# Kernel tuning notes

Hardware: AMD Instinct MI355X
Metric: run time of the kernel (lower is better)

The kernel has to match this reference:

```python
import jax, jax.numpy as jnp
import numpy as np

B, S, N = 128, 64, 32          # batch, self nodes, neighbors per node
INP_CAPS, OUT_CAPS, CAP_SZ = 8, 8, 16
K = OUT_CAPS
D = OUT_CAPS * CAP_SZ          # 128
C = D // K                     # capsule dim = 16
TAU = 1.0
EPS = 1e-12                    # F.normalize eps


def _l2norm(x):
    n = jnp.sqrt(jnp.sum(x * x, axis=-1, keepdims=True))
    return x / jnp.maximum(n, EPS)


def setup_inputs() -> dict:
    key = jax.random.key(0)
    k1, k2, k3, k4 = jax.random.split(key, 4)
    inp_d = INP_CAPS * CAP_SZ
    return {
        "self_vectors": jax.random.normal(k1, (B, S, inp_d), dtype=jnp.float32),
        "neighbor_vectors": jax.random.normal(k2, (B, S, N, inp_d), dtype=jnp.float32),
        "w1": jax.random.normal(k3, (inp_d, D), dtype=jnp.float32) * (1.0 / np.sqrt(inp_d)),
        "b1": jax.random.normal(k4, (D,), dtype=jnp.float32) * (1.0 / np.sqrt(D)),
        "max_iter": 3,
    }


def reference(self_vectors, neighbor_vectors, w1, b1, max_iter):
    inp_d = INP_CAPS * CAP_SZ
    self_z = jax.nn.relu(self_vectors.reshape(-1, inp_d) @ w1 + b1)
    neigh_z = jax.nn.relu(neighbor_vectors.reshape(-1, inp_d) @ w1 + b1)

    # [B,S,K,C] and [B,S,N,K,C], each capsule L2-normalized
    self_zn = _l2norm(self_z.reshape(B, S, K, C))
    neigh_zn = _l2norm(neigh_z.reshape(B, S, N, K, C))

    u = None
    for it in range(max_iter):
        if u is None:
            p = jnp.zeros((B, S, N, K), dtype=self_zn.dtype)
        else:
            # agreement scores: [B,S,N,K]
            p = jnp.einsum("bsnkc,bskc->bsnk", neigh_zn, u)
        p = jax.nn.softmax(p / TAU, axis=-1)
        # weighted neighbor sum over N -> [B,S,K,C]
        u = jnp.einsum("bsnkc,bsnk->bskc", neigh_zn, p) + self_zn
        if it < max_iter - 1:
            u = _l2norm(u)

    # dropout p=0.0 (eval) -> identity
    return jax.nn.relu(u.reshape(B, S, D))
```

## Files before the change

### kernel.cpp

```cpp
#include <hip/hip_runtime.h>
#include <hip/hip_bf16.h>


#define NB 32
#define DD 128
#define ZS 132
#define PPS 37
#define AST 136

#define SMEM_BYTES 20704
#define ALO_OFF_SH 4488
#define NRM_OFF_F 4488
#define PP_OFF_F 4752
#define UU_OFF_F 5048

typedef __attribute__((ext_vector_type(8))) short bf16x8;
typedef __attribute__((ext_vector_type(4))) float f32x4;
typedef __attribute__((ext_vector_type(4))) float float4v;
typedef __attribute__((ext_vector_type(2))) unsigned int uint2v;

__device__ __forceinline__ float bf16bits_to_f32(unsigned short u) {
  return __uint_as_float(((unsigned int)u) << 16);
}
__device__ __forceinline__ void split_bf16(float x, unsigned short& hi, unsigned short& lo) {
  unsigned int xb = __float_as_uint(x);
  hi = (unsigned short)(xb >> 16);
  float hif = __uint_as_float(xb & 0xFFFF0000u);
  float lof = x - hif;
  lo = (unsigned short)(__float_as_uint(lof) >> 16);
}

__global__ void detect_kernel(const unsigned short* __restrict__ w1u,
                              int* __restrict__ flag) {
  int t = threadIdx.x;
  float v = bf16bits_to_f32(w1u[2 * t]);
  int hit = !(fabsf(v) < 1e4f);
  unsigned long long m = __ballot(hit);
  if (t == 0) flag[0] = (m != 0ull) ? 1 : 0;
}

__global__ __launch_bounds__(256) void swizzle_w_kernel(
    const void* __restrict__ w1, const int* __restrict__ flag,
    unsigned short* __restrict__ whi, unsigned short* __restrict__ wlo) {
  int idx = blockIdx.x * 256 + threadIdx.x;
  int k = idx >> 7, n = idx & 127;
  int kt = k >> 5, q = (k >> 3) & 3, j = k & 7;
  int nt = n >> 4, nl = n & 15;
  int lane = q * 16 + nl;
  int dst = ((kt * 8 + nt) * 64 + lane) * 8 + j;
  unsigned short hb, lb;
  if (*flag) {
    split_bf16(((const float*)w1)[idx], hb, lb);
  } else {
    hb = ((const unsigned short*)w1)[idx];
    lb = 0;
  }
  whi[dst] = hb;
  wlo[dst] = lb;
}

__global__ __launch_bounds__(256) void routing_kernel(
    const void* __restrict__ selfv,
    const void* __restrict__ neighv,
    const unsigned short* __restrict__ whi,
    const unsigned short* __restrict__ wlo,
    const void* __restrict__ b1,
    void* __restrict__ out,
    const int* __restrict__ flag) {
  __shared__ __align__(16) unsigned char smem[SMEM_BYTES];
  unsigned short* Ahi = (unsigned short*)smem;
  unsigned short* Alo = Ahi + ALO_OFF_SH;
  float* zn = (float*)smem;
  float* nrm = (float*)smem + NRM_OFF_F;
  float* pp = (float*)smem + PP_OFF_F;
  float* uu = (float*)smem + UU_OFF_F;

  const int tid = threadIdx.x;
  const int lane = tid & 63;
  const int wv = tid >> 6;
  const int q = lane >> 4;
  const int ml = lane & 15;
  const size_t bs = blockIdx.x;
  const bool isf32 = (*flag != 0);

  const size_t noff = bs * (size_t)(NB * DD);
  const size_t soff = bs * (size_t)DD;

  if (isf32) {
    const float* nf = (const float*)neighv + noff;
    const float* sf = (const float*)selfv + soff;
#pragma unroll
    for (int i = 0; i < 4; ++i) {
      int f = tid + (i << 8);
      int r = f >> 5, c4 = f & 31;
      float4v v = ((const float4v*)nf)[f];
      unsigned short h0, h1, h2, h3, l0, l1, l2, l3;
      split_bf16(v[0], h0, l0);
      split_bf16(v[1], h1, l1);
      split_bf16(v[2], h2, l2);
      split_bf16(v[3], h3, l3);
      uint2v hw = (uint2v){(unsigned int)h0 | ((unsigned int)h1 << 16),
                           (unsigned int)h2 | ((unsigned int)h3 << 16)};
      uint2v lw = (uint2v){(unsigned int)l0 | ((unsigned int)l1 << 16),
                           (unsigned int)l2 | ((unsigned int)l3 << 16)};
      *(uint2v*)(Ahi + r * AST + c4 * 4) = hw;
      *(uint2v*)(Alo + r * AST + c4 * 4) = lw;
    }
    if (tid < 32) {
      float4v v = ((const float4v*)sf)[tid];
      unsigned short h0, h1, h2, h3, l0, l1, l2, l3;
      split_bf16(v[0], h0, l0);
      split_bf16(v[1], h1, l1);
      split_bf16(v[2], h2, l2);
      split_bf16(v[3], h3, l3);
      uint2v hw = (uint2v){(unsigned int)h0 | ((unsigned int)h1 << 16),
                           (unsigned int)h2 | ((unsigned int)h3 << 16)};
      uint2v lw = (uint2v){(unsigned int)l0 | ((unsigned int)l1 << 16),
                           (unsigned int)l2 | ((unsigned int)l3 << 16)};
      *(uint2v*)(Ahi + 32 * AST + tid * 4) = hw;
      *(uint2v*)(Alo + 32 * AST + tid * 4) = lw;
    }
  } else {
    const unsigned short* nbf = (const unsigned short*)neighv + noff;
    const unsigned short* sbf = (const unsigned short*)selfv + soff;
    const bf16x8 zv = (bf16x8){0, 0, 0, 0, 0, 0, 0, 0};
#pragma unroll
    for (int i = 0; i < 2; ++i) {
      int s = tid + (i << 8);
      int r = s >> 4, c8 = s & 15;
      bf16x8 v = *(const bf16x8*)(nbf + r * DD + c8 * 8);
      *(bf16x8*)(Ahi + r * AST + c8 * 8) = v;
      *(bf16x8*)(Alo + r * AST + c8 * 8) = zv;
    }
    if (tid < 16) {
      bf16x8 v = *(const bf16x8*)(sbf + tid * 8);
      *(bf16x8*)(Ahi + 32 * AST + tid * 8) = v;
      *(bf16x8*)(Alo + 32 * AST + tid * 8) = zv;
    }
  }
  __syncthreads();

  f32x4 acc[3][2];
#pragma unroll
  for (int mt = 0; mt < 3; ++mt)
#pragma unroll
    for (int jn = 0; jn < 2; ++jn) acc[mt][jn] = (f32x4){0.f, 0.f, 0.f, 0.f};

  const int nt0 = wv, nt1 = wv + 4;

#pragma unroll
  for (int kt = 0; kt < 4; ++kt) {
    const int fo = kt * 32 + q * 8;
    bf16x8 a0h = *(const bf16x8*)(Ahi + ml * AST + fo);
    bf16x8 a0l = *(const bf16x8*)(Alo + ml * AST + fo);
    bf16x8 a1h = *(const bf16x8*)(Ahi + (16 + ml) * AST + fo);
    bf16x8 a1l = *(const bf16x8*)(Alo + (16 + ml) * AST + fo);
    bf16x8 a2h = *(const bf16x8*)(Ahi + 32 * AST + fo);
    bf16x8 a2l = *(const bf16x8*)(Alo + 32 * AST + fo);
    const size_t bo0 = ((size_t)(kt * 8 + nt0) * 64 + lane) * 8;
    const size_t bo1 = ((size_t)(kt * 8 + nt1) * 64 + lane) * 8;
    bf16x8 b0h = *(const bf16x8*)(whi + bo0);
    bf16x8 b0l = *(const bf16x8*)(wlo + bo0);
    bf16x8 b1h = *(const bf16x8*)(whi + bo1);
    bf16x8 b1l = *(const bf16x8*)(wlo + bo1);

    acc[0][0] = __builtin_amdgcn_mfma_f32_16x16x32_bf16(a0h, b0h, acc[0][0], 0, 0, 0);
    acc[0][1] = __builtin_amdgcn_mfma_f32_16x16x32_bf16(a0h, b1h, acc[0][1], 0, 0, 0);
    acc[1][0] = __builtin_amdgcn_mfma_f32_16x16x32_bf16(a1h, b0h, acc[1][0], 0, 0, 0);
    acc[1][1] = __builtin_amdgcn_mfma_f32_16x16x32_bf16(a1h, b1h, acc[1][1], 0, 0, 0);
    acc[2][0] = __builtin_amdgcn_mfma_f32_16x16x32_bf16(a2h, b0h, acc[2][0], 0, 0, 0);
    acc[2][1] = __builtin_amdgcn_mfma_f32_16x16x32_bf16(a2h, b1h, acc[2][1], 0, 0, 0);
    acc[0][0] = __builtin_amdgcn_mfma_f32_16x16x32_bf16(a0h, b0l, acc[0][0], 0, 0, 0);
    acc[0][1] = __builtin_amdgcn_mfma_f32_16x16x32_bf16(a0h, b1l, acc[0][1], 0, 0, 0);
    acc[1][0] = __builtin_amdgcn_mfma_f32_16x16x32_bf16(a1h, b0l, acc[1][0], 0, 0, 0);
    acc[1][1] = __builtin_amdgcn_mfma_f32_16x16x32_bf16(a1h, b1l, acc[1][1], 0, 0, 0);
    acc[2][0] = __builtin_amdgcn_mfma_f32_16x16x32_bf16(a2h, b0l, acc[2][0], 0, 0, 0);
    acc[2][1] = __builtin_amdgcn_mfma_f32_16x16x32_bf16(a2h, b1l, acc[2][1], 0, 0, 0);
    acc[0][0] = __builtin_amdgcn_mfma_f32_16x16x32_bf16(a0l, b0h, acc[0][0], 0, 0, 0);
    acc[0][1] = __builtin_amdgcn_mfma_f32_16x16x32_bf16(a0l, b1h, acc[0][1], 0, 0, 0);
    acc[1][0] = __builtin_amdgcn_mfma_f32_16x16x32_bf16(a1l, b0h, acc[1][0], 0, 0, 0);
    acc[1][1] = __builtin_amdgcn_mfma_f32_16x16x32_bf16(a1l, b1h, acc[1][1], 0, 0, 0);
    acc[2][0] = __builtin_amdgcn_mfma_f32_16x16x32_bf16(a2l, b0h, acc[2][0], 0, 0, 0);
    acc[2][1] = __builtin_amdgcn_mfma_f32_16x16x32_bf16(a2l, b1h, acc[2][1], 0, 0, 0);
  }
  __syncthreads();

#pragma unroll
  for (int jn = 0; jn < 2; ++jn) {
    const int nt = jn ? nt1 : nt0;
    const int col = nt * 16 + ml;
    const float bias = isf32 ? ((const float*)b1)[col]
                             : bf16bits_to_f32(((const unsigned short*)b1)[col]);
#pragma unroll
    for (int mt = 0; mt < 3; ++mt) {
#pragma unroll
      for (int r = 0; r < 4; ++r) {
        const int row = mt * 16 + q * 4 + r;
        float v = fmaxf(acc[mt][jn][r] + bias, 0.f);
        if (row < 33) zn[row * ZS + col] = v;
      }
    }
  }
  __syncthreads();

  for (int id = tid; id < 264; id += 256) {
    const int row = id >> 3, k = id & 7;
    const float4v* zp = (const float4v*)&zn[row * ZS + k * 16];
    float4v a = zp[0], b = zp[1], c = zp[2], d = zp[3];
    float ss = a[0]*a[0]+a[1]*a[1]+a[2]*a[2]+a[3]*a[3]
             + b[0]*b[0]+b[1]*b[1]+b[2]*b[2]+b[3]*b[3]
             + c[0]*c[0]+c[1]*c[1]+c[2]*c[2]+c[3]*c[3]
             + d[0]*d[0]+d[1]*d[1]+d[2]*d[2]+d[3]*d[3];
    float nv = 1.f / fmaxf(sqrtf(ss), 1e-12f);
    nrm[id] = nv;
    if (row < 32) pp[k * PPS + row] = nv * 0.125f;
  }
  __syncthreads();

  const int k2 = tid >> 5, half = (tid >> 4) & 1, c2 = tid & 15;
  for (int it = 0; it < 3; ++it) {
    if (it > 0) {
      const int n1 = tid >> 3, k1 = tid & 7;
      const float4v* up = (const float4v*)&uu[k1 * 16];
      float4v u0 = up[0], u1 = up[1], u2 = up[2], u3 = up[3];
      const float4v* zp = (const float4v*)&zn[n1 * ZS + k1 * 16];
      float4v z0 = zp[0], z1 = zp[1], z2 = zp[2], z3 = zp[3];
      float dot = u0[0]*z0[0]+u0[1]*z0[1]+u0[2]*z0[2]+u0[3]*z0[3]
                + u1[0]*z1[0]+u1[1]*z1[1]+u1[2]*z1[2]+u1[3]*z1[3]
                + u2[0]*z2[0]+u2[1]*z2[1]+u2[2]*z2[2]+u2[3]*z2[3]
                + u3[0]*z3[0]+u3[1]*z3[1]+u3[2]*z3[2]+u3[3]*z3[3];
      const float nv = nrm[n1 * 8 + k1];
      float logit = dot * nv;
      float m = logit;
      m = fmaxf(m, __shfl_xor(m, 1));
      m = fmaxf(m, __shfl_xor(m, 2));
      m = fmaxf(m, __shfl_xor(m, 4));
      float e = __expf(logit - m);
      float s = e;
      s += __shfl_xor(s, 1);
      s += __shfl_xor(s, 2);
      s += __shfl_xor(s, 4);
      pp[k1 * PPS + n1] = (e / s) * nv;
      __syncthreads();
    }
    float s = 0.f;
#pragma unroll
    for (int n0 = 0; n0 < 16; ++n0) {
      const int n = half * 16 + n0;
      s += pp[k2 * PPS + n] * zn[n * ZS + k2 * 16 + c2];
    }
    s += __shfl_xor(s, 16);
    s += nrm[256 + k2] * zn[32 * ZS + k2 * 16 + c2];
    if (it < 2) {
      float ss = s * s;
      ss += __shfl_xor(ss, 1);
      ss += __shfl_xor(ss, 2);
      ss += __shfl_xor(ss, 4);
      ss += __shfl_xor(ss, 8);
      s *= 1.f / fmaxf(sqrtf(ss), 1e-12f);
      if (half == 0) uu[k2 * 16 + c2] = s;
    } else if (half == 0) {
      float r = (s < 0.f) ? 0.f : s;
      const size_t oidx = bs * DD + k2 * 16 + c2;
      if (isf32) {
        ((float*)out)[oidx] = r;
      } else {
        unsigned int xb = __float_as_uint(r);
        unsigned int l = (xb >> 16) & 1u;
        ((unsigned short*)out)[oidx] = (unsigned short)((xb + 0x7fffu + l) >> 16);
      }
    }
    __syncthreads();
  }
}

extern "C" void kernel_launch(void* const* d_in, const int* in_sizes, int n_in,
                              void* d_out, int out_size, void* d_ws, size_t ws_size,
                              hipStream_t stream) {
  (void)in_sizes; (void)n_in; (void)out_size; (void)ws_size;
  const void* selfv = d_in[0];
  const void* neighv = d_in[1];
  const void* w1 = d_in[2];
  const void* b1 = d_in[3];
  int* flag = (int*)d_ws;
  unsigned short* whi = (unsigned short*)((char*)d_ws + 64);
  unsigned short* wlo = (unsigned short*)((char*)d_ws + 64 + 32768);

  detect_kernel<<<1, 64, 0, stream>>>((const unsigned short*)w1, flag);
  swizzle_w_kernel<<<64, 256, 0, stream>>>(w1, flag, whi, wlo);
  routing_kernel<<<8192, 256, 0, stream>>>(selfv, neighv, whi, wlo, b1, d_out, flag);
}
```

Measured before the change: 238.8 us.

## Prefetch weight fragments, merge detect into swizzle, shrink shared memory

Folds the dtype-detection kernel into the weight swizzle kernel, which removes one launch. In the routing kernel, the first weight fragments and the bias are loaded before the barrier, and the next k-tile's weights are software-prefetched during the MFMA loop to hide global latency. The uu buffer is moved to overlap the dead Ahi/Alo area, which reduces shared memory, and launch bounds request 8 blocks per CU. The bf16 split now uses perm instructions for packing. The risks are extra register pressure from the prefetch and the occupancy hint, and possible aliasing errors from the overlapped uu region.

```diff
diff --git a/kernel.cpp b/kernel.cpp
--- a/kernel.cpp
+++ b/kernel.cpp
@@ -8,11 +8,11 @@
 #define PPS 37
 #define AST 136
 
-#define SMEM_BYTES 20704
+#define SMEM_BYTES 20192
 #define ALO_OFF_SH 4488
+#define UU_OFF_F 4352
 #define NRM_OFF_F 4488
 #define PP_OFF_F 4752
-#define UU_OFF_F 5048
 
 typedef __attribute__((ext_vector_type(8))) short bf16x8;
 typedef __attribute__((ext_vector_type(4))) float f32x4;
@@ -30,26 +30,47 @@
   lo = (unsigned short)(__float_as_uint(lof) >> 16);
 }
 
-__global__ void detect_kernel(const unsigned short* __restrict__ w1u,
-                              int* __restrict__ flag) {
+__device__ __forceinline__ void split4_store(float4v v, unsigned short* hp,
+                                             unsigned short* lp) {
+  unsigned int a = __float_as_uint(v[0]);
+  unsigned int b = __float_as_uint(v[1]);
+  unsigned int c = __float_as_uint(v[2]);
+  unsigned int d = __float_as_uint(v[3]);
+  unsigned int h01 = __builtin_amdgcn_perm(b, a, 0x07060302u);
+  unsigned int h23 = __builtin_amdgcn_perm(d, c, 0x07060302u);
+  unsigned int la = __float_as_uint(v[0] - __uint_as_float(a & 0xFFFF0000u));
+  unsigned int lb = __float_as_uint(v[1] - __uint_as_float(b & 0xFFFF0000u));
+  unsigned int lc = __float_as_uint(v[2] - __uint_as_float(c & 0xFFFF0000u));
+  unsigned int ld = __float_as_uint(v[3] - __uint_as_float(d & 0xFFFF0000u));
+  unsigned int l01 = __builtin_amdgcn_perm(lb, la, 0x07060302u);
+  unsigned int l23 = __builtin_amdgcn_perm(ld, lc, 0x07060302u);
+  *(uint2v*)hp = (uint2v){h01, h23};
+  *(uint2v*)lp = (uint2v){l01, l23};
+}
+
+__global__ __launch_bounds__(256) void swizzle_w_kernel(
+    const void* __restrict__ w1, int* __restrict__ flag,
+    unsigned short* __restrict__ whi, unsigned short* __restrict__ wlo) {
+  __shared__ int sflag;
   int t = threadIdx.x;
-  float v = bf16bits_to_f32(w1u[2 * t]);
-  int hit = !(fabsf(v) < 1e4f);
-  unsigned long long m = __ballot(hit);
-  if (t == 0) flag[0] = (m != 0ull) ? 1 : 0;
-}
-
-__global__ __launch_bounds__(256) void swizzle_w_kernel(
-    const void* __restrict__ w1, const int* __restrict__ flag,
-    unsigned short* __restrict__ whi, unsigned short* __restrict__ wlo) {
-  int idx = blockIdx.x * 256 + threadIdx.x;
+  if (t < 64) {
+    float v = bf16bits_to_f32(((const unsigned short*)w1)[2 * t]);
+    int hit = !(fabsf(v) < 1e4f);
+    unsigned long long m = __ballot(hit);
+    if (t == 0) sflag = (m != 0ull) ? 1 : 0;
+  }
+  __syncthreads();
+  const int isf = sflag;
+  if (blockIdx.x == 0 && t == 0) *flag = isf;
+
+  int idx = blockIdx.x * 256 + t;
   int k = idx >> 7, n = idx & 127;
   int kt = k >> 5, q = (k >> 3) & 3, j = k & 7;
   int nt = n >> 4, nl = n & 15;
   int lane = q * 16 + nl;
   int dst = ((kt * 8 + nt) * 64 + lane) * 8 + j;
   unsigned short hb, lb;
-  if (*flag) {
+  if (isf) {
     split_bf16(((const float*)w1)[idx], hb, lb);
   } else {
     hb = ((const unsigned short*)w1)[idx];
@@ -59,7 +80,7 @@
   wlo[dst] = lb;
 }
 
-__global__ __launch_bounds__(256) void routing_kernel(
+__global__ __launch_bounds__(256, 8) void routing_kernel(
     const void* __restrict__ selfv,
     const void* __restrict__ neighv,
     const unsigned short* __restrict__ whi,
@@ -71,9 +92,9 @@
   unsigned short* Ahi = (unsigned short*)smem;
   unsigned short* Alo = Ahi + ALO_OFF_SH;
   float* zn = (float*)smem;
+  float* uu = (float*)smem + UU_OFF_F;
   float* nrm = (float*)smem + NRM_OFF_F;
   float* pp = (float*)smem + PP_OFF_F;
-  float* uu = (float*)smem + UU_OFF_F;
 
   const int tid = threadIdx.x;
   const int lane = tid & 63;
@@ -94,31 +115,11 @@
       int f = tid + (i << 8);
       int r = f >> 5, c4 = f & 31;
       float4v v = ((const float4v*)nf)[f];
-      unsigned short h0, h1, h2, h3, l0, l1, l2, l3;
-      split_bf16(v[0], h0, l0);
-      split_bf16(v[1], h1, l1);
-      split_bf16(v[2], h2, l2);
-      split_bf16(v[3], h3, l3);
-      uint2v hw = (uint2v){(unsigned int)h0 | ((unsigned int)h1 << 16),
-                           (unsigned int)h2 | ((unsigned int)h3 << 16)};
-      uint2v lw = (uint2v){(unsigned int)l0 | ((unsigned int)l1 << 16),
-                           (unsigned int)l2 | ((unsigned int)l3 << 16)};
-      *(uint2v*)(Ahi + r * AST + c4 * 4) = hw;
-      *(uint2v*)(Alo + r * AST + c4 * 4) = lw;
+      split4_store(v, Ahi + r * AST + c4 * 4, Alo + r * AST + c4 * 4);
     }
     if (tid < 32) {
       float4v v = ((const float4v*)sf)[tid];
-      unsigned short h0, h1, h2, h3, l0, l1, l2, l3;
-      split_bf16(v[0], h0, l0);
-      split_bf16(v[1], h1, l1);
-      split_bf16(v[2], h2, l2);
-      split_bf16(v[3], h3, l3);
-      uint2v hw = (uint2v){(unsigned int)h0 | ((unsigned int)h1 << 16),
-                           (unsigned int)h2 | ((unsigned int)h3 << 16)};
-      uint2v lw = (uint2v){(unsigned int)l0 | ((unsigned int)l1 << 16),
-                           (unsigned int)l2 | ((unsigned int)l3 << 16)};
-      *(uint2v*)(Ahi + 32 * AST + tid * 4) = hw;
-      *(uint2v*)(Alo + 32 * AST + tid * 4) = lw;
+      split4_store(v, Ahi + 32 * AST + tid * 4, Alo + 32 * AST + tid * 4);
     }
   } else {
     const unsigned short* nbf = (const unsigned short*)neighv + noff;
@@ -138,6 +139,22 @@
       *(bf16x8*)(Alo + 32 * AST + tid * 8) = zv;
     }
   }
+
+  const int nt0 = wv, nt1 = wv + 4;
+  size_t bo0 = ((size_t)(0 * 8 + nt0) * 64 + lane) * 8;
+  size_t bo1 = ((size_t)(0 * 8 + nt1) * 64 + lane) * 8;
+  bf16x8 nb0h = *(const bf16x8*)(whi + bo0);
+  bf16x8 nb0l = *(const bf16x8*)(wlo + bo0);
+  bf16x8 nb1h = *(const bf16x8*)(whi + bo1);
+  bf16x8 nb1l = *(const bf16x8*)(wlo + bo1);
+  float bias0, bias1;
+  if (isf32) {
+    bias0 = ((const float*)b1)[nt0 * 16 + ml];
+    bias1 = ((const float*)b1)[nt1 * 16 + ml];
+  } else {
+    bias0 = bf16bits_to_f32(((const unsigned short*)b1)[nt0 * 16 + ml]);
+    bias1 = bf16bits_to_f32(((const unsigned short*)b1)[nt1 * 16 + ml]);
+  }
   __syncthreads();
 
   f32x4 acc[3][2];
@@ -146,10 +163,17 @@
 #pragma unroll
     for (int jn = 0; jn < 2; ++jn) acc[mt][jn] = (f32x4){0.f, 0.f, 0.f, 0.f};
 
-  const int nt0 = wv, nt1 = wv + 4;
-
 #pragma unroll
   for (int kt = 0; kt < 4; ++kt) {
+    bf16x8 b0h = nb0h, b0l = nb0l, b1h = nb1h, b1l = nb1l;
+    if (kt < 3) {
+      const size_t pbo0 = ((size_t)((kt + 1) * 8 + nt0) * 64 + lane) * 8;
+      const size_t pbo1 = ((size_t)((kt + 1) * 8 + nt1) * 64 + lane) * 8;
+      nb0h = *(const bf16x8*)(whi + pbo0);
+      nb0l = *(const bf16x8*)(wlo + pbo0);
+      nb1h = *(const bf16x8*)(whi + pbo1);
+      nb1l = *(const bf16x8*)(wlo + pbo1);
+    }
     const int fo = kt * 32 + q * 8;
     bf16x8 a0h = *(const bf16x8*)(Ahi + ml * AST + fo);
     bf16x8 a0l = *(const bf16x8*)(Alo + ml * AST + fo);
@@ -157,12 +181,6 @@
     bf16x8 a1l = *(const bf16x8*)(Alo + (16 + ml) * AST + fo);
     bf16x8 a2h = *(const bf16x8*)(Ahi + 32 * AST + fo);
     bf16x8 a2l = *(const bf16x8*)(Alo + 32 * AST + fo);
-    const size_t bo0 = ((size_t)(kt * 8 + nt0) * 64 + lane) * 8;
-    const size_t bo1 = ((size_t)(kt * 8 + nt1) * 64 + lane) * 8;
-    bf16x8 b0h = *(const bf16x8*)(whi + bo0);
-    bf16x8 b0l = *(const bf16x8*)(wlo + bo0);
-    bf16x8 b1h = *(const bf16x8*)(whi + bo1);
-    bf16x8 b1l = *(const bf16x8*)(wlo + bo1);
 
     acc[0][0] = __builtin_amdgcn_mfma_f32_16x16x32_bf16(a0h, b0h, acc[0][0], 0, 0, 0);
     acc[0][1] = __builtin_amdgcn_mfma_f32_16x16x32_bf16(a0h, b1h, acc[0][1], 0, 0, 0);
@@ -189,8 +207,7 @@
   for (int jn = 0; jn < 2; ++jn) {
     const int nt = jn ? nt1 : nt0;
     const int col = nt * 16 + ml;
-    const float bias = isf32 ? ((const float*)b1)[col]
-                             : bf16bits_to_f32(((const unsigned short*)b1)[col]);
+    const float bias = jn ? bias1 : bias0;
 #pragma unroll
     for (int mt = 0; mt < 3; ++mt) {
 #pragma unroll
@@ -286,7 +303,6 @@
   unsigned short* whi = (unsigned short*)((char*)d_ws + 64);
   unsigned short* wlo = (unsigned short*)((char*)d_ws + 64 + 32768);
 
-  detect_kernel<<<1, 64, 0, stream>>>((const unsigned short*)w1, flag);
   swizzle_w_kernel<<<64, 256, 0, stream>>>(w1, flag, whi, wlo);
   routing_kernel<<<8192, 256, 0, stream>>>(selfv, neighv, whi, wlo, b1, d_out, flag);
 }
```

After: 219.8 us. 8.0% less time.
